# Optimization experiments

Measured on AMD Instinct MI355X. Metric: run time of the kernel, lower is better.

## Reference

```python
import jax, jax.numpy as jnp
import numpy as np

EMBED_DIM = 32
HIDDEN_DIM = 64
N = 1024
LN_EPS = 1e-5


def setup_inputs() -> dict:
    key = jax.random.key(0)
    ks = jax.random.split(key, 8)
    d, h = EMBED_DIM, HIDDEN_DIM
    s1 = 1.0 / np.sqrt(2 * d)
    s2 = 1.0 / np.sqrt(h)
    return {
        "node_embeddings": jax.random.normal(ks[0], (N, d), dtype=jnp.float32),
        # Linear(2d -> h), stored as (2d, h) for x @ W
        "W1": jax.random.uniform(ks[1], (2 * d, h), jnp.float32, -s1, s1),
        "b1": jnp.zeros((h,), jnp.float32),
        "g1": jnp.ones((h,), jnp.float32),
        "be1": jnp.zeros((h,), jnp.float32),
        "W2": jax.random.uniform(ks[2], (h, h), jnp.float32, -s2, s2),
        "b2": jnp.zeros((h,), jnp.float32),
        "g2": jnp.ones((h,), jnp.float32),
        "be2": jnp.zeros((h,), jnp.float32),
        "W3": jax.random.uniform(ks[3], (h, 1), jnp.float32, -s2, s2),
        "b3": jnp.zeros((1,), jnp.float32),
    }


def _layernorm(x, gamma, beta):
    mu = jnp.mean(x, axis=-1, keepdims=True)
    var = jnp.mean(jnp.square(x - mu), axis=-1, keepdims=True)
    return (x - mu) * jax.lax.rsqrt(var + LN_EPS) * gamma + beta


def reference(node_embeddings, W1, b1, g1, be1, W2, b2, g2, be2, W3, b3):
    n, d = node_embeddings.shape
    # pair_emb = cat([src_emb, dst_emb], -1); first linear applied without
    # materializing the concat: split W1 into src/dst halves.
    W1s, W1d = W1[:d], W1[d:]
    hs = node_embeddings @ W1s          # (N, h)
    hd = node_embeddings @ W1d          # (N, h)
    h = hs[:, None, :] + hd[None, :, :] + b1   # (N, N, h)
    h = jax.nn.relu(_layernorm(h, g1, be1))
    h = jax.nn.relu(_layernorm(h @ W2 + b2, g2, be2))
    out = jax.nn.sigmoid((h @ W3 + b3)[..., 0])  # (N, N)
    return out
```

## Files before the change

kernel.cpp:

```cpp
#include <hip/hip_runtime.h>
#include <hip/hip_bf16.h>

#define NN 1024
#define ED 32
#define HD 64
#define LN_EPS 1e-5f

typedef short bf16x8 __attribute__((ext_vector_type(8)));
typedef float f32x4 __attribute__((ext_vector_type(4)));

#define OFF_HS   0
#define OFF_HDB  65536
#define OFF_SS   131072
#define OFF_SD   132096
#define OFF_G1   133120
#define OFF_BE1  133184
#define OFF_B2   133248
#define OFF_G2   133312
#define OFF_BE2  133376
#define OFF_W3   133440
#define OFF_B3   133504
#define OFF_SB2  133505
#define OFF_W2F  133508

__device__ __forceinline__ bool buf_is_f32(const void* g1) {
  return *(const unsigned int*)g1 == 0x3F800000u;
}
template <bool F32>
__device__ __forceinline__ float ld(const void* p, int i) {
  return F32 ? ((const float*)p)[i]
             : __bfloat162float(((const __hip_bfloat16*)p)[i]);
}
__device__ __forceinline__ unsigned short f2bf(float f) {
  unsigned int b = __builtin_bit_cast(unsigned int, f);
  b += 0x7FFFu + ((b >> 16) & 1u);
  return (unsigned short)(b >> 16);
}
__device__ __forceinline__ unsigned int pack2bf(float a, float b) {
  return (unsigned int)f2bf(a) | ((unsigned int)f2bf(b) << 16);
}
__device__ __forceinline__ unsigned int pk_bf(float a, float b) {
  __hip_bfloat162 p = __float22bfloat162_rn(make_float2(a, b));
  unsigned int u;
  __builtin_memcpy(&u, &p, 4);
  return u;
}
__device__ __forceinline__ f32x4 splat4(float v) { f32x4 r = {v, v, v, v}; return r; }

template <int CTRL>
__device__ __forceinline__ float dpp_add(float v) {
  int m = __builtin_amdgcn_update_dpp(0, __builtin_bit_cast(int, v), CTRL, 0xF, 0xF, true);
  return v + __builtin_bit_cast(float, m);
}
template <int CTRL>
__device__ __forceinline__ float dpp_mov(float v) {
  return __builtin_bit_cast(float,
      __builtin_amdgcn_update_dpp(0, __builtin_bit_cast(int, v), CTRL, 0xF, 0xF, true));
}
__device__ __forceinline__ float red16(float v) {
  v = dpp_add<0xB1>(v);
  v = dpp_add<0x4E>(v);
  v = dpp_add<0x124>(v);
  v = dpp_add<0x128>(v);
  return v;
}

template <bool F32>
__device__ void prep_body(const void* E, const void* W1, const void* b1,
                          const void* g1, const void* be1, const void* W2,
                          const void* b2, const void* g2, const void* be2,
                          const void* W3, const void* b3, float* ws) {
  const int i = blockIdx.x, t = threadIdx.x;
  if (i < NN) {
    __shared__ float e[ED];
    if (t < ED) e[t] = ld<F32>(E, i * ED + t);
    __syncthreads();
    int k = t & 63;
    bool dside = t >= 64;
    int wofs = dside ? ED * HD : 0;
    float acc = 0.f;
#pragma unroll
    for (int c = 0; c < ED; ++c)
      acc = fmaf(e[c], ld<F32>(W1, wofs + c * HD + k), acc);
    if (dside) acc += ld<F32>(b1, k);
    float s = acc;
#pragma unroll
    for (int m = 1; m <= 32; m <<= 1) s += __shfl_xor(s, m);
    if (dside) {
      ws[OFF_HDB + i * HD + k] = acc;
      if (k == 0) ws[OFF_SD + i] = s;
    } else {
      ws[OFF_HS + i * HD + k] = acc;
      if (k == 0) ws[OFF_SS + i] = s;
    }
  } else if (i < NN + 16) {
    if (t < 32) {
      int d = (i - NN) * 32 + t;
      int lv = d & 63, nt = (d >> 6) & 3, kc = d >> 8;
      int k0 = kc * 32 + ((lv >> 4) & 3) * 8;
      int n = nt * 16 + (lv & 15);
      unsigned int u4[4];
#pragma unroll
      for (int jj = 0; jj < 4; ++jj)
        u4[jj] = pack2bf(ld<F32>(W2, (k0 + 2 * jj) * HD + n),
                         ld<F32>(W2, (k0 + 2 * jj + 1) * HD + n));
      ((uint4*)(ws + OFF_W2F))[d] = make_uint4(u4[0], u4[1], u4[2], u4[3]);
    }
  } else {
    __shared__ float rs[64];
    if (t < 64) {
      ws[OFF_G1  + t] = ld<F32>(g1,  t);
      ws[OFF_BE1 + t] = ld<F32>(be1, t);
      ws[OFF_B2  + t] = ld<F32>(b2,  t);
      ws[OFF_G2  + t] = ld<F32>(g2,  t);
      ws[OFF_BE2 + t] = ld<F32>(be2, t);
      ws[OFF_W3  + t] = ld<F32>(W3,  t);
      float s = 0.f;
      for (int n = 0; n < HD; ++n) s += ld<F32>(W2, t * HD + n);
      rs[t] = s;
    }
    if (t == 64) {
      float s = 0.f;
      for (int n = 0; n < HD; ++n) s += ld<F32>(b2, n);
      ws[OFF_SB2] = s;
    }
    if (t == 65) ws[OFF_B3] = ld<F32>(b3, 0);
    __syncthreads();
    unsigned short* st = (unsigned short*)(ws + OFF_W2F) + 4096;
    for (int s = t; s < 1024; s += 128) {
      int j = s & 7, lv = (s >> 3) & 63, kc = s >> 9;
      st[s] = f2bf(rs[kc * 32 + ((lv >> 4) & 3) * 8 + j]);
    }
  }
}

__global__ __launch_bounds__(128) void prep_kern(
    const void* E, const void* W1, const void* b1, const void* g1,
    const void* be1, const void* W2, const void* b2, const void* g2,
    const void* be2, const void* W3, const void* b3, float* ws) {
  if (buf_is_f32(g1))
    prep_body<true >(E, W1, b1, g1, be1, W2, b2, g2, be2, W3, b3, ws);
  else
    prep_body<false>(E, W1, b1, g1, be1, W2, b2, g2, be2, W3, b3, ws);
}

__global__ __launch_bounds__(256, 4) void pair_kern(
    const float* __restrict__ ws, float* __restrict__ out) {
  __shared__ float sh[1024];
  __shared__ float sdt[1024];
  __shared__ __align__(16) unsigned int X[256 * 32];
  const int t = threadIdx.x;
  const int bid = blockIdx.x;
  const int lid = (bid & 7) * 512 + (bid >> 3);
  const int bi = lid >> 6, bj = lid & 63;
  const int l = t & 63, w = t >> 6;
  const int q = l >> 4, ln = l & 15;
  const int il = t >> 4, jl = t & 15;
  const float inv = 1.f / 64.f;

  {
    int r = t >> 4, c4 = t & 15;
    ((f32x4*)sh )[r * 16 + (c4 ^ r)] = ((const f32x4*)(ws + OFF_HS  + (bi * 16 + r) * HD))[c4];
    ((f32x4*)sdt)[r * 16 + (c4 ^ r)] = ((const f32x4*)(ws + OFF_HDB + (bj * 16 + r) * HD))[c4];
  }
  const float ssum = ws[OFF_SS + bi * 16 + il];
  const float dsum = ws[OFF_SD + bj * 16 + jl];
  float b2v[4], g2v[4], be2v[4], w3v[4];
#pragma unroll
  for (int nt = 0; nt < 4; ++nt) {
    int cix = nt * 16 + ln;
    b2v[nt]  = ws[OFF_B2  + cix];
    g2v[nt]  = ws[OFF_G2  + cix];
    be2v[nt] = ws[OFF_BE2 + cix];
    w3v[nt]  = ws[OFF_W3  + cix];
  }
  const float b3s = ws[OFF_B3];
  const float Sb2 = ws[OFF_SB2];
  __syncthreads();

  {
    const f32x4* A4 = (const f32x4*)sh;
    const f32x4* B4 = (const f32x4*)sdt;
    f32x4 xv[16];
    f32x4 q4 = splat4(0.f);
#pragma unroll
    for (int c = 0; c < 16; ++c) {
      f32x4 x = A4[il * 16 + (c ^ il)] + B4[jl * 16 + (c ^ jl)];
      xv[c] = x;
      q4 = __builtin_elementwise_fma(x, x, q4);
    }
    float ssq = (q4[0] + q4[1]) + (q4[2] + q4[3]);
    float mu = (ssum + dsum) * inv;
    float r1 = rsqrtf(fmaf(-mu, mu, ssq * inv) + LN_EPS);
    f32x4 r1v = splat4(r1), nm = splat4(-mu * r1), zero = splat4(0.f);
    uint4* Xr4 = (uint4*)(X + t * 32);
#pragma unroll
    for (int b = 0; b < 8; ++b) {
      unsigned int uu[4];
#pragma unroll
      for (int h = 0; h < 2; ++h) {
        int c = 2 * b + h;
        f32x4 g, be;
#pragma unroll
        for (int e = 0; e < 4; ++e) {
          g[e]  = ws[OFF_G1  + c * 4 + e];
          be[e] = ws[OFF_BE1 + c * 4 + e];
        }
        f32x4 u = __builtin_elementwise_fma(xv[c], r1v, nm);
        f32x4 v = __builtin_elementwise_fma(u, g, be);
        v = __builtin_elementwise_max(v, zero);
        uu[2 * h]     = pk_bf(v[0], v[1]);
        uu[2 * h + 1] = pk_bf(v[2], v[3]);
      }
      Xr4[b ^ (t & 7)] = make_uint4(uu[0], uu[1], uu[2], uu[3]);
    }
  }

  bf16x8 bf[2][4], bsum[2];
  const uint4* WF4 = (const uint4*)(ws + OFF_W2F);
#pragma unroll
  for (int kc = 0; kc < 2; ++kc) {
#pragma unroll
    for (int nt = 0; nt < 4; ++nt)
      bf[kc][nt] = __builtin_bit_cast(bf16x8, WF4[(kc * 4 + nt) * 64 + l]);
    bsum[kc] = __builtin_bit_cast(bf16x8, WF4[512 + kc * 64 + l]);
  }
  const uint4* XL = (const uint4*)X;
  float zp[16];
#pragma unroll
  for (int mt = 0; mt < 4; ++mt) {
    int m = w * 64 + mt * 16 + ln;
    bf16x8 a0 = __builtin_bit_cast(bf16x8, XL[m * 8 + (q ^ (m & 7))]);
    bf16x8 a1 = __builtin_bit_cast(bf16x8, XL[m * 8 + ((q + 4) ^ (m & 7))]);
    f32x4 acc5[5];
#pragma unroll
    for (int nt = 0; nt < 5; ++nt) {
      bf16x8 b0  = (nt < 4) ? bf[0][nt] : bsum[0];
      bf16x8 b1f = (nt < 4) ? bf[1][nt] : bsum[1];
      f32x4 z4 = splat4(nt < 4 ? b2v[nt] : Sb2);
      z4 = __builtin_amdgcn_mfma_f32_16x16x32_bf16(a0, b0, z4, 0, 0, 0);
      acc5[nt] = __builtin_amdgcn_mfma_f32_16x16x32_bf16(a1, b1f, z4, 0, 0, 0);
    }
    f32x4 qq = splat4(0.f);
#pragma unroll
    for (int nt = 0; nt < 4; ++nt)
      qq = __builtin_elementwise_fma(acc5[nt], acc5[nt], qq);
#pragma unroll
    for (int e = 0; e < 4; ++e) qq[e] = red16(qq[e]);
    f32x4 mu = acc5[4] * splat4(inv);
    f32x4 var = __builtin_elementwise_fma(qq, splat4(inv), -(mu * mu));
    f32x4 r2;
#pragma unroll
    for (int e = 0; e < 4; ++e) r2[e] = rsqrtf(var[e] + LN_EPS);
    f32x4 nm2 = -(mu * r2);
    f32x4 z4 = splat4(0.f);
#pragma unroll
    for (int nt = 0; nt < 4; ++nt) {
      f32x4 u = __builtin_elementwise_fma(acc5[nt], r2, nm2);
      f32x4 v = __builtin_elementwise_fma(u, splat4(g2v[nt]), splat4(be2v[nt]));
      v = __builtin_elementwise_max(v, splat4(0.f));
      z4 = __builtin_elementwise_fma(v, splat4(w3v[nt]), z4);
    }
#pragma unroll
    for (int e = 0; e < 4; ++e) zp[mt * 4 + e] = z4[e];
  }

  const bool p8 = (l & 8) != 0, p4b = (l & 4) != 0;
  const bool p2b = (l & 2) != 0, p1b = (l & 1) != 0;
  float s8v[8];
#pragma unroll
  for (int j = 0; j < 8; ++j) {
    float kept = p8 ? zp[j + 8] : zp[j];
    float disc = p8 ? zp[j] : zp[j + 8];
    s8v[j] = kept + dpp_mov<0x128>(disc);
  }
  float s4v[4];
#pragma unroll
  for (int j = 0; j < 4; ++j) {
    float kept = p4b ? s8v[j + 4] : s8v[j];
    float disc = p4b ? s8v[j] : s8v[j + 4];
    s4v[j] = kept + dpp_mov<0x141>(disc);
  }
  float s2v[2];
#pragma unroll
  for (int j = 0; j < 2; ++j) {
    float kept = p2b ? s4v[j + 2] : s4v[j];
    float disc = p2b ? s4v[j] : s4v[j + 2];
    s2v[j] = kept + dpp_mov<0x4E>(disc);
  }
  {
    float kept = p1b ? s2v[1] : s2v[0];
    float disc = p1b ? s2v[0] : s2v[1];
    float zfin = kept + dpp_mov<0xB1>(disc);
    float o = 1.f / (1.f + __expf(-(zfin + b3s)));
    out[(bi * 16 + w * 4 + (ln >> 2)) * NN + bj * 16 + q * 4 + (ln & 3)] = o;
  }
}

extern "C" void kernel_launch(void* const* d_in, const int* in_sizes, int n_in,
                              void* d_out, int out_size, void* d_ws, size_t ws_size,
                              hipStream_t stream) {
  float* ws = (float*)d_ws;
  hipLaunchKernelGGL(prep_kern, dim3(NN + 17), dim3(128), 0, stream,
                     d_in[0], d_in[1], d_in[2], d_in[3], d_in[4], d_in[5],
                     d_in[6], d_in[7], d_in[8], d_in[9], d_in[10], ws);
  hipLaunchKernelGGL(pair_kern, dim3(4096), dim3(256), 0, stream,
                     ws, (float*)d_out);
}
```

Measured before the change: 134.2 us.

## Recompute LN1 inputs from LDS and reduce per-tile outputs incrementally to cut registers

Stops holding the 16 f32x4 pre-norm values in registers across the LayerNorm-1 statistics pass and instead re-reads and re-adds them from shared memory when normalizing. The final 16-lane DPP reduction is also restructured so that partial sums are folded after each M tile, rather than keeping 16 values live until the end. The output index mapping is changed to match the new reduction order. Together these lower VGPR pressure to allow higher occupancy, at the cost of extra LDS reads and adds.

```diff
diff --git a/kernel.cpp b/kernel.cpp
--- a/kernel.cpp
+++ b/kernel.cpp
@@ -165,6 +165,61 @@
   }
   const float ssum = ws[OFF_SS + bi * 16 + il];
   const float dsum = ws[OFF_SD + bj * 16 + jl];
+  __syncthreads();
+
+  const f32x4* A4 = (const f32x4*)sh;
+  const f32x4* B4 = (const f32x4*)sdt;
+
+  float r1, nmu;
+  {
+    f32x4 q4 = splat4(0.f);
+#pragma unroll
+    for (int c = 0; c < 16; ++c) {
+      f32x4 x = A4[il * 16 + (c ^ il)] + B4[jl * 16 + (c ^ jl)];
+      q4 = __builtin_elementwise_fma(x, x, q4);
+    }
+    float ssq = (q4[0] + q4[1]) + (q4[2] + q4[3]);
+    float mu = (ssum + dsum) * inv;
+    r1 = rsqrtf(fmaf(-mu, mu, ssq * inv) + LN_EPS);
+    nmu = -mu * r1;
+  }
+  asm volatile("" ::: "memory");
+
+  {
+    f32x4 r1v = splat4(r1), nm = splat4(nmu), zero = splat4(0.f);
+    uint4* Xr4 = (uint4*)(X + t * 32);
+#pragma unroll
+    for (int b = 0; b < 8; ++b) {
+      unsigned int uu[4];
+#pragma unroll
+      for (int h = 0; h < 2; ++h) {
+        int c = 2 * b + h;
+        f32x4 x = A4[il * 16 + (c ^ il)] + B4[jl * 16 + (c ^ jl)];
+        f32x4 g, be;
+#pragma unroll
+        for (int e = 0; e < 4; ++e) {
+          g[e]  = ws[OFF_G1  + c * 4 + e];
+          be[e] = ws[OFF_BE1 + c * 4 + e];
+        }
+        f32x4 u = __builtin_elementwise_fma(x, r1v, nm);
+        f32x4 v = __builtin_elementwise_fma(u, g, be);
+        v = __builtin_elementwise_max(v, zero);
+        uu[2 * h]     = pk_bf(v[0], v[1]);
+        uu[2 * h + 1] = pk_bf(v[2], v[3]);
+      }
+      Xr4[b ^ (t & 7)] = make_uint4(uu[0], uu[1], uu[2], uu[3]);
+    }
+  }
+
+  bf16x8 bf[2][4], bsum[2];
+  const uint4* WF4 = (const uint4*)(ws + OFF_W2F);
+#pragma unroll
+  for (int kc = 0; kc < 2; ++kc) {
+#pragma unroll
+    for (int nt = 0; nt < 4; ++nt)
+      bf[kc][nt] = __builtin_bit_cast(bf16x8, WF4[(kc * 4 + nt) * 64 + l]);
+    bsum[kc] = __builtin_bit_cast(bf16x8, WF4[512 + kc * 64 + l]);
+  }
   float b2v[4], g2v[4], be2v[4], w3v[4];
 #pragma unroll
   for (int nt = 0; nt < 4; ++nt) {
@@ -176,57 +231,11 @@
   }
   const float b3s = ws[OFF_B3];
   const float Sb2 = ws[OFF_SB2];
-  __syncthreads();
-
-  {
-    const f32x4* A4 = (const f32x4*)sh;
-    const f32x4* B4 = (const f32x4*)sdt;
-    f32x4 xv[16];
-    f32x4 q4 = splat4(0.f);
-#pragma unroll
-    for (int c = 0; c < 16; ++c) {
-      f32x4 x = A4[il * 16 + (c ^ il)] + B4[jl * 16 + (c ^ jl)];
-      xv[c] = x;
-      q4 = __builtin_elementwise_fma(x, x, q4);
-    }
-    float ssq = (q4[0] + q4[1]) + (q4[2] + q4[3]);
-    float mu = (ssum + dsum) * inv;
-    float r1 = rsqrtf(fmaf(-mu, mu, ssq * inv) + LN_EPS);
-    f32x4 r1v = splat4(r1), nm = splat4(-mu * r1), zero = splat4(0.f);
-    uint4* Xr4 = (uint4*)(X + t * 32);
-#pragma unroll
-    for (int b = 0; b < 8; ++b) {
-      unsigned int uu[4];
-#pragma unroll
-      for (int h = 0; h < 2; ++h) {
-        int c = 2 * b + h;
-        f32x4 g, be;
-#pragma unroll
-        for (int e = 0; e < 4; ++e) {
-          g[e]  = ws[OFF_G1  + c * 4 + e];
-          be[e] = ws[OFF_BE1 + c * 4 + e];
-        }
-        f32x4 u = __builtin_elementwise_fma(xv[c], r1v, nm);
-        f32x4 v = __builtin_elementwise_fma(u, g, be);
-        v = __builtin_elementwise_max(v, zero);
-        uu[2 * h]     = pk_bf(v[0], v[1]);
-        uu[2 * h + 1] = pk_bf(v[2], v[3]);
-      }
-      Xr4[b ^ (t & 7)] = make_uint4(uu[0], uu[1], uu[2], uu[3]);
-    }
-  }
-
-  bf16x8 bf[2][4], bsum[2];
-  const uint4* WF4 = (const uint4*)(ws + OFF_W2F);
-#pragma unroll
-  for (int kc = 0; kc < 2; ++kc) {
-#pragma unroll
-    for (int nt = 0; nt < 4; ++nt)
-      bf[kc][nt] = __builtin_bit_cast(bf16x8, WF4[(kc * 4 + nt) * 64 + l]);
-    bsum[kc] = __builtin_bit_cast(bf16x8, WF4[512 + kc * 64 + l]);
-  }
+
   const uint4* XL = (const uint4*)X;
-  float zp[16];
+  const bool pb0 = (l & 1) != 0, pb1 = (l & 2) != 0;
+  const bool pb2 = (l & 4) != 0, pb3 = (l & 8) != 0;
+  float zq[4];
 #pragma unroll
   for (int mt = 0; mt < 4; ++mt) {
     int m = w * 64 + mt * 16 + ln;
@@ -261,40 +270,23 @@
       v = __builtin_elementwise_max(v, splat4(0.f));
       z4 = __builtin_elementwise_fma(v, splat4(w3v[nt]), z4);
     }
-#pragma unroll
-    for (int e = 0; e < 4; ++e) zp[mt * 4 + e] = z4[e];
-  }
-
-  const bool p8 = (l & 8) != 0, p4b = (l & 4) != 0;
-  const bool p2b = (l & 2) != 0, p1b = (l & 1) != 0;
-  float s8v[8];
-#pragma unroll
-  for (int j = 0; j < 8; ++j) {
-    float kept = p8 ? zp[j + 8] : zp[j];
-    float disc = p8 ? zp[j] : zp[j + 8];
-    s8v[j] = kept + dpp_mov<0x128>(disc);
-  }
-  float s4v[4];
-#pragma unroll
-  for (int j = 0; j < 4; ++j) {
-    float kept = p4b ? s8v[j + 4] : s8v[j];
-    float disc = p4b ? s8v[j] : s8v[j + 4];
-    s4v[j] = kept + dpp_mov<0x141>(disc);
-  }
-  float s2v[2];
-#pragma unroll
-  for (int j = 0; j < 2; ++j) {
-    float kept = p2b ? s4v[j + 2] : s4v[j];
-    float disc = p2b ? s4v[j] : s4v[j + 2];
-    s2v[j] = kept + dpp_mov<0x4E>(disc);
-  }
-  {
-    float kept = p1b ? s2v[1] : s2v[0];
-    float disc = p1b ? s2v[0] : s2v[1];
-    float zfin = kept + dpp_mov<0xB1>(disc);
-    float o = 1.f / (1.f + __expf(-(zfin + b3s)));
-    out[(bi * 16 + w * 4 + (ln >> 2)) * NN + bj * 16 + q * 4 + (ln & 3)] = o;
-  }
+    float ka0 = pb3 ? z4[2] : z4[0], da0 = pb3 ? z4[0] : z4[2];
+    float ka1 = pb3 ? z4[3] : z4[1], da1 = pb3 ? z4[1] : z4[3];
+    float za0 = ka0 + dpp_mov<0x128>(da0);
+    float za1 = ka1 + dpp_mov<0x128>(da1);
+    float kb = pb2 ? za1 : za0, db = pb2 ? za0 : za1;
+    zq[mt] = kb + dpp_mov<0x141>(db);
+  }
+
+  float kc0 = pb1 ? zq[2] : zq[0], dc0 = pb1 ? zq[0] : zq[2];
+  float kc1 = pb1 ? zq[3] : zq[1], dc1 = pb1 ? zq[1] : zq[3];
+  float zc0 = kc0 + dpp_mov<0x4E>(dc0);
+  float zc1 = kc1 + dpp_mov<0x4E>(dc1);
+  float kd = pb0 ? zc1 : zc0, dd = pb0 ? zc0 : zc1;
+  float zfin = kd + dpp_mov<0xB1>(dd);
+
+  float o = 1.f / (1.f + __expf(-(zfin + b3s)));
+  out[(bi * 16 + w * 4 + (l & 3)) * NN + bj * 16 + q * 4 + ((l >> 2) & 3)] = o;
 }
 
 extern "C" void kernel_launch(void* const* d_in, const int* in_sizes, int n_in,
```

Result: faster. 112.8 us (-16.0%).
